# Kernel optimization log

Measured on AMD Instinct MI355X. Metric: run time of the kernel, lower is better.

Reference implementation:

```python
import jax, jax.numpy as jnp
import numpy as np
from jax import lax

B, C, H0, W0 = 8, 128, 62, 62
G, K, DIL, STRIDE, PAD = 4, 3, 1, 1, 1
P = K * K
GC = C // G
OFFSET_SCALE = 1.0


def setup_inputs() -> dict:
    key = jax.random.key(0)
    ks = jax.random.split(key, 10)
    s = 0.05
    return {
        "x": jax.random.normal(ks[0], (B, C, H0, W0), jnp.float32),
        "conv_w": jax.random.normal(ks[1], (C, C, 1, 1), jnp.float32) * s,
        "conv_b": jax.random.normal(ks[2], (C,), jnp.float32) * s,
        "in_proj_w": jax.random.normal(ks[3], (C, C), jnp.float32) * s,
        "in_proj_b": jnp.zeros((C,), jnp.float32),
        "dw_w": jax.random.normal(ks[4], (C, 1, K, K), jnp.float32) * s,
        "dw_b": jnp.zeros((C,), jnp.float32),
        "ln_g": jnp.ones((C,), jnp.float32),
        "ln_b": jnp.zeros((C,), jnp.float32),
        "off_w": jax.random.normal(ks[5], (C, G * P * 2), jnp.float32) * s,
        "off_b": jax.random.normal(ks[6], (G * P * 2,), jnp.float32) * s,
        "mask_w": jax.random.normal(ks[7], (C, G * P), jnp.float32) * s,
        "mask_b": jnp.zeros((G * P,), jnp.float32),
        "out_proj_w": jax.random.normal(ks[8], (C, C), jnp.float32) * s,
        "out_proj_b": jnp.zeros((C,), jnp.float32),
    }


def _bilinear_sample(img, ix, iy, Hp, Wp):
    # img: [B, G, Hp*Wp, GC] flattened spatial; ix, iy: [B, G, Q, P] pixel coords.
    # Matches torch grid_sample(bilinear, zeros, align_corners=False).
    x0 = jnp.floor(ix)
    y0 = jnp.floor(iy)

    def gather(xi, yi):
        valid = (xi >= 0) & (xi <= Wp - 1) & (yi >= 0) & (yi <= Hp - 1)
        xc = jnp.clip(xi, 0, Wp - 1).astype(jnp.int32)
        yc = jnp.clip(yi, 0, Hp - 1).astype(jnp.int32)
        lin = (yc * Wp + xc).reshape(img.shape[0], img.shape[1], -1)  # [B,G,Q*P]
        v = jnp.take_along_axis(img, lin[..., None], axis=2)          # [B,G,Q*P,GC]
        v = v.reshape(xi.shape + (img.shape[-1],))
        return v * valid[..., None].astype(img.dtype)

    wx1 = (ix - x0)[..., None]
    wx0 = 1.0 - wx1
    wy1 = (iy - y0)[..., None]
    wy0 = 1.0 - wy1
    return (gather(x0, y0) * wx0 * wy0
            + gather(x0 + 1.0, y0) * wx1 * wy0
            + gather(x0, y0 + 1.0) * wx0 * wy1
            + gather(x0 + 1.0, y0 + 1.0) * wx1 * wy1)


def _dcnv3_core(x_proj, offset, mask):
    # x_proj: [B,H,W,C] NHWC; offset: [B,H,W,G*P*2]; mask: [B,H,W,G*P] (softmaxed)
    Bn, H, W, _ = x_proj.shape
    xp = jnp.pad(x_proj, ((0, 0), (PAD, PAD), (PAD, PAD), (0, 0)))
    Hp, Wp = H + 2 * PAD, W + 2 * PAD  # H_out == H for K=3, PAD=1, STRIDE=1
    # reference points (normalized to padded size)
    ref_x = (jnp.arange(W, dtype=jnp.float32) * STRIDE + (DIL * (K - 1)) / 2.0 + 0.5) / Wp
    ref_y = (jnp.arange(H, dtype=jnp.float32) * STRIDE + (DIL * (K - 1)) / 2.0 + 0.5) / Hp
    ref = jnp.stack(jnp.broadcast_arrays(ref_x[None, :], ref_y[:, None]), -1)  # [H,W,2] (x,y)
    # dilation grid (same ordering as torch.meshgrid(x_lin, y_lin))
    klin = (jnp.arange(K, dtype=jnp.float32) * DIL - (DIL * (K - 1)) // 2)
    gx, gy = jnp.meshgrid(klin, klin, indexing='ij')
    grid = jnp.stack([gx / Wp, gy / Hp], -1).reshape(P, 2)
    grid = jnp.tile(grid[None], (G, 1, 1)).reshape(G * P, 2)
    spatial_norm = jnp.array([Wp, Hp], jnp.float32)
    loc = (ref[:, :, None, :] + grid[None, None] * OFFSET_SCALE)[None] \
        + offset.reshape(Bn, H, W, G * P, 2) * OFFSET_SCALE / spatial_norm
    g = 2.0 * loc - 1.0  # normalized grid in [-1,1]
    ix = ((g[..., 0] + 1.0) * Wp - 1.0) / 2.0  # align_corners=False unnormalize
    iy = ((g[..., 1] + 1.0) * Hp - 1.0) / 2.0
    Q = H * W
    ix = ix.reshape(Bn, Q, G, P).transpose(0, 2, 1, 3)  # [B,G,Q,P]
    iy = iy.reshape(Bn, Q, G, P).transpose(0, 2, 1, 3)
    img = xp.reshape(Bn, Hp * Wp, G, GC).transpose(0, 2, 1, 3)  # [B,G,S,GC]
    sampled = _bilinear_sample(img, ix, iy, Hp, Wp)             # [B,G,Q,P,GC]
    m = mask.reshape(Bn, Q, G, P).transpose(0, 2, 1, 3)
    out = jnp.einsum('bgqpc,bgqp->bqgc', sampled, m)
    return out.reshape(Bn, H, W, G * GC)


def reference(x, conv_w, conv_b, in_proj_w, in_proj_b, dw_w, dw_b, ln_g, ln_b,
              off_w, off_b, mask_w, mask_b, out_proj_w, out_proj_b):
    dn = ('NCHW', 'OIHW', 'NCHW')
    # 1x1 conv with padding=1 (spatial grows by 2 on each dim)
    y = lax.conv_general_dilated(x, conv_w, (1, 1), ((PAD, PAD), (PAD, PAD)),
                                 dimension_numbers=dn) + conv_b[None, :, None, None]
    t = y.transpose(0, 2, 3, 1)  # NHWC
    x_proj = t @ in_proj_w + in_proj_b
    # offset/mask branch: depthwise conv + LayerNorm + GELU
    d = lax.conv_general_dilated(y, dw_w, (1, 1), ((1, 1), (1, 1)),
                                 dimension_numbers=dn,
                                 feature_group_count=C) + dw_b[None, :, None, None]
    d = d.transpose(0, 2, 3, 1)
    mu = d.mean(-1, keepdims=True)
    var = ((d - mu) ** 2).mean(-1, keepdims=True)
    d = (d - mu) / jnp.sqrt(var + 1e-5) * ln_g + ln_b
    d = jax.nn.gelu(d, approximate=False)
    offset = d @ off_w + off_b
    Bn, H, W, _ = d.shape
    m = jax.nn.softmax((d @ mask_w + mask_b).reshape(Bn, H, W, G, P), axis=-1)
    out = _dcnv3_core(x_proj, offset, m.reshape(Bn, H, W, G * P))
    out = out @ out_proj_w + out_proj_b
    return out.transpose(0, 3, 1, 2)  # back to NCHW
```

## Files before the change

kernel.cpp:

```cpp
#include <hip/hip_runtime.h>
#include <math.h>

#define BB 8
#define CH 128
#define HH 64
#define WWID 64
#define HIN 62
#define WIN 62
#define SPIN (HIN*WIN)
#define HP 66
#define WP 66
#define GP2 70
#define GG 4
#define GCH 32
#define NPIX (BB*HH*WWID)
#define ASTRIDE 136
#define XPHALFS ((size_t)BB*GP2*GP2*CH)

typedef _Float16 v8h __attribute__((ext_vector_type(8)));
typedef _Float16 v4h __attribute__((ext_vector_type(4)));
typedef float    v4f __attribute__((ext_vector_type(4)));
typedef float    f4a __attribute__((ext_vector_type(4), aligned(4)));

__global__ __launch_bounds__(256) void p0_pack(const float* __restrict__ conv_w,
                                               const float* __restrict__ in_proj_w,
                                               const float* __restrict__ off_w,
                                               const float* __restrict__ mask_w,
                                               const float* __restrict__ out_proj_w,
                                               const float* __restrict__ dw_w,
                                               _Float16* __restrict__ wp,
                                               float* __restrict__ dwT,
                                               _Float16* __restrict__ xpad16) {
    int t = threadIdx.x;
    int blk = blockIdx.x;
    if (blk >= 32) {
        size_t nvec = XPHALFS / 8;
        for (size_t i = (size_t)(blk - 32) * 256 + t; i < nvec; i += 32 * 256)
            *(v8h*)&xpad16[i * 8] = (v8h)(_Float16)0;
        return;
    }
    if (blk == 31) {
        if (t < 128) {
            #pragma unroll
            for (int tap = 0; tap < 9; tap++) dwT[tap * 128 + t] = dw_w[t * 9 + tap];
        }
        return;
    }
    int tid = blk * 256 + t;
    int mat, base;
    if (tid < 2048)      { mat = 0; base = 0; }
    else if (tid < 4096) { mat = 1; base = 2048; }
    else if (tid < 5888) { mat = 2; base = 4096; }
    else                 { mat = 3; base = 5888; }
    int fi = tid - base;
    int nt = fi >> 8, rem = fi & 255, kc = rem >> 6, lane = rem & 63;
    int n = nt * 16 + (lane & 15);
    int kbase = kc * 32 + ((lane >> 4) & 3) * 8;
    _Float16* dst = wp + (size_t)tid * 8;
    #pragma unroll
    for (int j = 0; j < 8; j++) {
        int k = kbase + j;
        float v;
        if (mat == 0)      v = conv_w[n * CH + k];
        else if (mat == 1) v = in_proj_w[k * CH + n];
        else if (mat == 2) v = (n < 72) ? off_w[k * 72 + n]
                               : (n < 108 ? mask_w[k * 36 + (n - 72)] : 0.f);
        else               v = out_proj_w[k * CH + n];
        dst[j] = (_Float16)v;
    }
}

__device__ inline void mfma_loop8(const _Float16* __restrict__ a16,
                                  const _Float16* __restrict__ wp,
                                  v4f acc[4], int t) {
    int lane = t & 63;
    int wv = t >> 6;
    int mt = wv >> 1, ntb = (wv & 1) * 4;
    const _Float16* abase = a16 + (mt * 16 + (lane & 15)) * ASTRIDE + ((lane >> 4) * 8);
    #pragma unroll
    for (int kc = 0; kc < 4; kc++) {
        v8h av = *(const v8h*)(abase + kc * 32);
        #pragma unroll
        for (int j = 0; j < 4; j++) {
            v8h bv = *(const v8h*)(wp + ((size_t)((ntb + j) * 4 + kc) * 64 + lane) * 8);
            acc[j] = __builtin_amdgcn_mfma_f32_16x16x32_f16(av, bv, acc[j], 0, 0, 0);
        }
    }
}

__device__ inline void acc_to_a16_8(_Float16* a16, v4f acc[4], int t) {
    int lane = t & 63, ncol = lane & 15;
    int wv = t >> 6;
    int m0 = (wv >> 1) * 16 + ((lane >> 4) * 4);
    int ntb = (wv & 1) * 4;
    #pragma unroll
    for (int j = 0; j < 4; j++)
        #pragma unroll
        for (int r = 0; r < 4; r++)
            a16[(m0 + r) * ASTRIDE + (ntb + j) * 16 + ncol] = (_Float16)acc[j][r];
}

__global__ __launch_bounds__(512) void gA_conv_inproj(const float* __restrict__ x,
                                                      const _Float16* __restrict__ wp_conv,
                                                      const _Float16* __restrict__ wp_in,
                                                      const float* __restrict__ conv_b,
                                                      const float* __restrict__ in_b,
                                                      _Float16* __restrict__ y16,
                                                      _Float16* __restrict__ xpad16) {
    __shared__ _Float16 a16[64 * ASTRIDE];
    int pix0 = blockIdx.x * 64;
    int t = threadIdx.x;
    int h = (pix0 >> 6) & 63, b = pix0 >> 12;
    bool hin = (h >= 1 && h <= 62);
    for (int q = t; q < 2048; q += 512) {
        int c = q >> 4, w4 = (q & 15) * 4;
        float4 v = make_float4(0.f, 0.f, 0.f, 0.f);
        if (hin) {
            const float* xr = x + ((size_t)(b * CH + c)) * SPIN + (h - 1) * WIN;
            if (w4 == 0)       { f4a e = *(const f4a*)&xr[0];      v = make_float4(0.f, e[0], e[1], e[2]); }
            else if (w4 == 60) { f4a e = *(const f4a*)&xr[58];     v = make_float4(e[1], e[2], e[3], 0.f); }
            else               { f4a e = *(const f4a*)&xr[w4 - 1]; v = make_float4(e[0], e[1], e[2], e[3]); }
        }
        a16[(w4 + 0) * ASTRIDE + c] = (_Float16)v.x;
        a16[(w4 + 1) * ASTRIDE + c] = (_Float16)v.y;
        a16[(w4 + 2) * ASTRIDE + c] = (_Float16)v.z;
        a16[(w4 + 3) * ASTRIDE + c] = (_Float16)v.w;
    }
    __syncthreads();
    int lane = t & 63, ncol = lane & 15;
    int ntb = ((t >> 6) & 1) * 4;
    v4f acc[4];
    #pragma unroll
    for (int j = 0; j < 4; j++) {
        float bv = conv_b[(ntb + j) * 16 + ncol];
        acc[j] = (v4f){bv, bv, bv, bv};
    }
    mfma_loop8(a16, wp_conv, acc, t);
    __syncthreads();
    acc_to_a16_8(a16, acc, t);
    __syncthreads();
    {
        _Float16* dst = y16 + (size_t)pix0 * CH;
        for (int q = t; q < 1024; q += 512)
            *(v8h*)&dst[q * 8] = *(const v8h*)&a16[(q >> 4) * ASTRIDE + (q & 15) * 8];
    }
    v4f acc2[4];
    #pragma unroll
    for (int j = 0; j < 4; j++) {
        float bv = in_b[(ntb + j) * 16 + ncol];
        acc2[j] = (v4f){bv, bv, bv, bv};
    }
    mfma_loop8(a16, wp_in, acc2, t);
    __syncthreads();
    acc_to_a16_8(a16, acc2, t);
    __syncthreads();
    {
        _Float16* dst = xpad16 + (size_t)(((b * GP2) + h + 3) * GP2 + 3) * CH;
        for (int q = t; q < 1024; q += 512)
            *(v8h*)&dst[q * 8] = *(const v8h*)&a16[(q >> 4) * ASTRIDE + (q & 15) * 8];
    }
}

__global__ __launch_bounds__(512) void gF_dwln_offmask(const _Float16* __restrict__ y16,
                                                       const _Float16* __restrict__ wp_om,
                                                       const float* __restrict__ dwT,
                                                       const float* __restrict__ dw_b,
                                                       const float* __restrict__ ln_g,
                                                       const float* __restrict__ ln_b,
                                                       const float* __restrict__ off_b,
                                                       const float* __restrict__ mask_b,
                                                       float* __restrict__ tapmeta) {
    __shared__ char smem[49920];
    _Float16* ylds = (_Float16*)smem;
    int t = threadIdx.x;
    int pix0 = blockIdx.x * 64;
    int h = (pix0 >> 6) & 63, b = pix0 >> 12;
    if (h == 0 || h == 63) {
        for (int i = t; i < 3120; i += 512) *(v8h*)&ylds[i * 8] = (v8h)(_Float16)0;
        __syncthreads();
    }
    for (int idx = t; idx < 3072; idx += 512) {
        int r = idx >> 10, w = (idx >> 4) & 63, c8 = idx & 15;
        int hh = h + r - 1;
        if (hh >= 0 && hh <= 63) {
            v8h v = *(const v8h*)&y16[(size_t)(((b * 64 + hh) * 64 + w) * CH) + c8 * 8];
            *(v8h*)&ylds[(size_t)((r * 16 + c8) * 65 + w) * 8] = v;
        }
    }
    __syncthreads();
    int px = t >> 3, q8 = t & 7;
    float acc[16];
    #pragma unroll
    for (int cb = 0; cb < 4; cb++) *(float4*)&acc[cb * 4] = *(const float4*)&dw_b[q8 * 16 + cb * 4];
    #pragma unroll
    for (int r = 0; r < 3; r++) {
        #pragma unroll
        for (int kx = 0; kx < 3; kx++) {
            int wq = px + kx - 1;
            bool valid = (wq >= 0 && wq <= 63);
            int wpc = min(max(wq, 0), 63);
            int tap = r * 3 + kx;
            if (valid) {
                #pragma unroll
                for (int cb = 0; cb < 2; cb++) {
                    v8h yv = *(const v8h*)&ylds[(size_t)((r * 16 + q8 * 2 + cb) * 65 + wpc) * 8];
                    float4 wa = *(const float4*)&dwT[tap * 128 + q8 * 16 + cb * 8];
                    float4 wb = *(const float4*)&dwT[tap * 128 + q8 * 16 + cb * 8 + 4];
                    acc[cb*8+0] += (float)yv[0] * wa.x; acc[cb*8+1] += (float)yv[1] * wa.y;
                    acc[cb*8+2] += (float)yv[2] * wa.z; acc[cb*8+3] += (float)yv[3] * wa.w;
                    acc[cb*8+4] += (float)yv[4] * wb.x; acc[cb*8+5] += (float)yv[5] * wb.y;
                    acc[cb*8+6] += (float)yv[6] * wb.z; acc[cb*8+7] += (float)yv[7] * wb.w;
                }
            }
        }
    }
    float s = 0.f, ss = 0.f;
    #pragma unroll
    for (int j = 0; j < 16; j++) { s += acc[j]; ss += acc[j] * acc[j]; }
    s  += __shfl_xor(s, 1);  s  += __shfl_xor(s, 2);  s  += __shfl_xor(s, 4);
    ss += __shfl_xor(ss, 1); ss += __shfl_xor(ss, 2); ss += __shfl_xor(ss, 4);
    float mu = s * (1.f / 128.f);
    float var = ss * (1.f / 128.f) - mu * mu;
    float rstd = rsqrtf(var + 1e-5f);
    v8h dreg[2];
    #pragma unroll
    for (int cb = 0; cb < 2; cb++) {
        float4 ga = *(const float4*)&ln_g[q8 * 16 + cb * 8];
        float4 gb = *(const float4*)&ln_g[q8 * 16 + cb * 8 + 4];
        float4 ba = *(const float4*)&ln_b[q8 * 16 + cb * 8];
        float4 bb = *(const float4*)&ln_b[q8 * 16 + cb * 8 + 4];
        float gv[8] = {ga.x, ga.y, ga.z, ga.w, gb.x, gb.y, gb.z, gb.w};
        float bv[8] = {ba.x, ba.y, ba.z, ba.w, bb.x, bb.y, bb.z, bb.w};
        #pragma unroll
        for (int j = 0; j < 8; j++) {
            float xln = (acc[cb * 8 + j] - mu) * rstd * gv[j] + bv[j];
            float gel = 0.5f * xln * (1.f + erff(xln * 0.70710678118654752f));
            dreg[cb][j] = (_Float16)gel;
        }
    }
    __syncthreads();
    _Float16* a16 = (_Float16*)smem;
    float* om = (float*)(smem + 17408);
    #pragma unroll
    for (int cb = 0; cb < 2; cb++)
        *(v8h*)&a16[px * ASTRIDE + q8 * 16 + cb * 8] = dreg[cb];
    __syncthreads();
    int lane = t & 63, ncol = lane & 15;
    int ntb = ((t >> 6) & 1) * 4;
    v4f macc[4];
    #pragma unroll
    for (int j = 0; j < 4; j++) {
        int n = (ntb + j) * 16 + ncol;
        float bv = (n < 72) ? off_b[n] : (n < 108 ? mask_b[n - 72] : 0.f);
        macc[j] = (v4f){bv, bv, bv, bv};
    }
    mfma_loop8(a16, wp_om, macc, t);
    int m0 = ((t >> 6) >> 1) * 16 + ((lane >> 4) * 4);
    #pragma unroll
    for (int j = 0; j < 4; j++) {
        if (ntb + j < 7) {
            #pragma unroll
            for (int r = 0; r < 4; r++)
                om[(m0 + r) * 112 + (ntb + j) * 16 + ncol] = macc[j][r];
        }
    }
    __syncthreads();
    {
        int job = t >> 1, half = t & 1;
        int pxs = job >> 2, gx = job & 3;
        const float* row = &om[pxs * 112];
        float lg[9];
        #pragma unroll
        for (int i = 0; i < 9; i++) lg[i] = row[72 + gx * 9 + i];
        float mx = lg[0];
        #pragma unroll
        for (int i = 1; i < 9; i++) mx = fmaxf(mx, lg[i]);
        float e[9], sum = 0.f;
        #pragma unroll
        for (int i = 0; i < 9; i++) { e[i] = expf(lg[i] - mx); sum += e[i]; }
        float inv = 1.f / sum;
        float* tm = tapmeta + ((size_t)(pix0 + pxs) * 36 + gx * 9) * 4;
        int pstart = half * 5;
        int pcount = half ? 4 : 5;
        #pragma unroll
        for (int pp = 0; pp < 5; pp++) {
            if (pp >= pcount) break;
            int p = pstart + pp;
            int gp = gx * 9 + p;
            float offx = row[gp * 2];
            float offy = row[gp * 2 + 1];
            float m = e[p] * inv;
            float ix = (float)(pxs + (p / 3)) + offx;
            float iy = (float)(h + (p % 3)) + offy;
            ix = fminf(fmaxf(ix, -2.f), (float)(WP + 1));
            iy = fminf(fmaxf(iy, -2.f), (float)(HP + 1));
            float x0f = floorf(ix), y0f = floorf(iy);
            float fx = ix - x0f, fy = iy - y0f;
            int x0 = (int)x0f, y0 = (int)y0f;
            int off = ((y0 + 2) * GP2 + (x0 + 2)) * CH;
            float4 rec;
            rec.x = __int_as_float(off);
            rec.y = fx; rec.z = fy; rec.w = m;
            *(float4*)&tm[p * 4] = rec;
        }
    }
}

__global__ __launch_bounds__(256) void kD_gather(const _Float16* __restrict__ xpad16,
                                                 const float* __restrict__ tapmeta,
                                                 _Float16* __restrict__ core16) {
    __shared__ float meta[8 * 36 * 4];
    int t = threadIdx.x;
    int pix0 = blockIdx.x * 8;
    const float4* src = (const float4*)(tapmeta + (size_t)pix0 * 36 * 4);
    for (int i = t; i < 288; i += 256) ((float4*)meta)[i] = src[i];
    __syncthreads();
    int px_l = t >> 5, lane5 = t & 31;
    int c4 = lane5 * 4, g = lane5 >> 3;
    int pix = pix0 + px_l;
    int b = pix >> 12;
    const _Float16* base = xpad16 + (size_t)b * GP2 * GP2 * CH + c4;
    float a0 = 0.f, a1 = 0.f, a2 = 0.f, a3 = 0.f;
    #pragma unroll
    for (int p = 0; p < 9; p++) {
        float4 rec = *(const float4*)&meta[(size_t)(px_l * 36 + g * 9 + p) * 4];
        int off = __float_as_int(rec.x);
        float fx = rec.y, fy = rec.z, m = rec.w;
        float w11 = fx * fy;
        float w10 = fx - w11;
        float w01 = fy - w11;
        float w00 = 1.f - fx - fy + w11;
        w00 *= m; w10 *= m; w01 *= m; w11 *= m;
        v4h h0 = *(const v4h*)&base[off];
        v4h h1 = *(const v4h*)&base[off + CH];
        v4h h2 = *(const v4h*)&base[off + GP2 * CH];
        v4h h3 = *(const v4h*)&base[off + GP2 * CH + CH];
        a0 += w00*(float)h0[0] + w10*(float)h1[0] + w01*(float)h2[0] + w11*(float)h3[0];
        a1 += w00*(float)h0[1] + w10*(float)h1[1] + w01*(float)h2[1] + w11*(float)h3[1];
        a2 += w00*(float)h0[2] + w10*(float)h1[2] + w01*(float)h2[2] + w11*(float)h3[2];
        a3 += w00*(float)h0[3] + w10*(float)h1[3] + w01*(float)h2[3] + w11*(float)h3[3];
    }
    v4h res = { (_Float16)a0, (_Float16)a1, (_Float16)a2, (_Float16)a3 };
    *(v4h*)&core16[(size_t)pix * CH + c4] = res;
}

__global__ __launch_bounds__(512) void g4_outproj(const _Float16* __restrict__ core16,
                                                  const _Float16* __restrict__ wp,
                                                  const float* __restrict__ bias,
                                                  float* __restrict__ out) {
    __shared__ _Float16 a16[64 * ASTRIDE];
    __shared__ float res[128 * 68];
    int pix0 = blockIdx.x * 64;
    int t = threadIdx.x;
    const _Float16* src = core16 + (size_t)pix0 * CH;
    for (int q = t; q < 1024; q += 512)
        *(v8h*)&a16[(q >> 4) * ASTRIDE + (q & 15) * 8] = *(const v8h*)&src[q * 8];
    __syncthreads();
    int lane = t & 63, ncol = lane & 15;
    int ntb = ((t >> 6) & 1) * 4;
    v4f acc[4];
    #pragma unroll
    for (int j = 0; j < 4; j++) {
        float bv = bias[(ntb + j) * 16 + ncol];
        acc[j] = (v4f){bv, bv, bv, bv};
    }
    mfma_loop8(a16, wp, acc, t);
    int m0 = ((t >> 6) >> 1) * 16 + ((lane >> 4) * 4);
    #pragma unroll
    for (int j = 0; j < 4; j++)
        #pragma unroll
        for (int r = 0; r < 4; r++)
            res[((ntb + j) * 16 + ncol) * 68 + (m0 + r)] = acc[j][r];
    __syncthreads();
    int b = pix0 >> 12, h = (pix0 >> 6) & 63;
    for (int q = t; q < 2048; q += 512) {
        int cc = q >> 4, w4 = (q & 15) * 4;
        float4 o = *(const float4*)&res[cc * 68 + w4];
        *(float4*)&out[(size_t)((b * CH + cc) * HH + h) * WWID + w4] = o;
    }
}

extern "C" void kernel_launch(void* const* d_in, const int* in_sizes, int n_in,
                              void* d_out, int out_size, void* d_ws, size_t ws_size,
                              hipStream_t stream) {
    const float* x        = (const float*)d_in[0];
    const float* conv_w   = (const float*)d_in[1];
    const float* conv_b   = (const float*)d_in[2];
    const float* in_proj_w= (const float*)d_in[3];
    const float* in_proj_b= (const float*)d_in[4];
    const float* dw_w     = (const float*)d_in[5];
    const float* dw_b     = (const float*)d_in[6];
    const float* ln_g     = (const float*)d_in[7];
    const float* ln_b     = (const float*)d_in[8];
    const float* off_w    = (const float*)d_in[9];
    const float* off_b    = (const float*)d_in[10];
    const float* mask_w   = (const float*)d_in[11];
    const float* mask_b   = (const float*)d_in[12];
    const float* out_proj_w = (const float*)d_in[13];
    const float* out_proj_b = (const float*)d_in[14];
    float* out = (float*)d_out;

    float* ws = (float*)d_ws;
    const size_t O_WP   = 0;
    const size_t O_DWT  = 32768;
    const size_t O_Y16  = 34816;
    const size_t O_XP16 = O_Y16 + 2097152;
    const size_t O_C16  = O_XP16 + 2508800;
    const size_t O_TM   = O_C16 + 2097152;
    _Float16* wp     = (_Float16*)(ws + O_WP);
    float*    dwT    = ws + O_DWT;
    _Float16* y16    = (_Float16*)(ws + O_Y16);
    _Float16* xpad16 = (_Float16*)(ws + O_XP16);
    _Float16* core16 = (_Float16*)(ws + O_C16);
    float*    tapmeta= ws + O_TM;

    _Float16* wp_conv = wp;
    _Float16* wp_in   = wp + (size_t)2048 * 8;
    _Float16* wp_om   = wp + (size_t)4096 * 8;
    _Float16* wp_out  = wp + (size_t)5888 * 8;

    p0_pack<<<64, 256, 0, stream>>>(conv_w, in_proj_w, off_w, mask_w, out_proj_w, dw_w, wp, dwT, xpad16);
    gA_conv_inproj<<<NPIX / 64, 512, 0, stream>>>(x, wp_conv, wp_in, conv_b, in_proj_b, y16, xpad16);
    gF_dwln_offmask<<<NPIX / 64, 512, 0, stream>>>(y16, wp_om, dwT, dw_b, ln_g, ln_b, off_b, mask_b, tapmeta);
    kD_gather<<<NPIX / 8, 256, 0, stream>>>(xpad16, tapmeta, core16);
    g4_outproj<<<NPIX / 64, 512, 0, stream>>>(core16, wp_out, out_proj_b, out);
}
```

Baseline: 162.7 us.

## Fuse deformable gather with output projection in one kernel

Merges the bilinear gather kernel and the out-projection MFMA kernel into one kernel that handles 16 pixels per 128-thread block. The sampled core values stay in shared memory as fp16 and feed the MFMA directly, so the core16 intermediate is never written to or read back from global memory and one launch disappears. Each thread now gathers 16 channels with 8-wide vector loads instead of 4, which cuts the number of load instructions. In exchange, each block reloads the full out-projection weights for only 16 pixels, and the output stores become 64-byte row segments rather than full 256-byte rows.

```diff
diff --git a/kernel.cpp b/kernel.cpp
--- a/kernel.cpp
+++ b/kernel.cpp
@@ -306,77 +306,93 @@
     }
 }
 
-__global__ __launch_bounds__(256) void kD_gather(const _Float16* __restrict__ xpad16,
-                                                 const float* __restrict__ tapmeta,
-                                                 _Float16* __restrict__ core16) {
-    __shared__ float meta[8 * 36 * 4];
+__global__ __launch_bounds__(128) void gG_gather_outproj(const _Float16* __restrict__ xpad16,
+                                                         const float* __restrict__ tapmeta,
+                                                         const _Float16* __restrict__ wp,
+                                                         const float* __restrict__ bias,
+                                                         float* __restrict__ out) {
+    __shared__ char smem[14592];
+    _Float16* a16 = (_Float16*)smem;
+    float* meta = (float*)(smem + 4352);
+    float* res  = (float*)(smem + 4352);
     int t = threadIdx.x;
-    int pix0 = blockIdx.x * 8;
-    const float4* src = (const float4*)(tapmeta + (size_t)pix0 * 36 * 4);
-    for (int i = t; i < 288; i += 256) ((float4*)meta)[i] = src[i];
-    __syncthreads();
-    int px_l = t >> 5, lane5 = t & 31;
-    int c4 = lane5 * 4, g = lane5 >> 3;
-    int pix = pix0 + px_l;
-    int b = pix >> 12;
-    const _Float16* base = xpad16 + (size_t)b * GP2 * GP2 * CH + c4;
-    float a0 = 0.f, a1 = 0.f, a2 = 0.f, a3 = 0.f;
-    #pragma unroll
-    for (int p = 0; p < 9; p++) {
-        float4 rec = *(const float4*)&meta[(size_t)(px_l * 36 + g * 9 + p) * 4];
-        int off = __float_as_int(rec.x);
-        float fx = rec.y, fy = rec.z, m = rec.w;
-        float w11 = fx * fy;
-        float w10 = fx - w11;
-        float w01 = fy - w11;
-        float w00 = 1.f - fx - fy + w11;
-        w00 *= m; w10 *= m; w01 *= m; w11 *= m;
-        v4h h0 = *(const v4h*)&base[off];
-        v4h h1 = *(const v4h*)&base[off + CH];
-        v4h h2 = *(const v4h*)&base[off + GP2 * CH];
-        v4h h3 = *(const v4h*)&base[off + GP2 * CH + CH];
-        a0 += w00*(float)h0[0] + w10*(float)h1[0] + w01*(float)h2[0] + w11*(float)h3[0];
-        a1 += w00*(float)h0[1] + w10*(float)h1[1] + w01*(float)h2[1] + w11*(float)h3[1];
-        a2 += w00*(float)h0[2] + w10*(float)h1[2] + w01*(float)h2[2] + w11*(float)h3[2];
-        a3 += w00*(float)h0[3] + w10*(float)h1[3] + w01*(float)h2[3] + w11*(float)h3[3];
-    }
-    v4h res = { (_Float16)a0, (_Float16)a1, (_Float16)a2, (_Float16)a3 };
-    *(v4h*)&core16[(size_t)pix * CH + c4] = res;
-}
-
-__global__ __launch_bounds__(512) void g4_outproj(const _Float16* __restrict__ core16,
-                                                  const _Float16* __restrict__ wp,
-                                                  const float* __restrict__ bias,
-                                                  float* __restrict__ out) {
-    __shared__ _Float16 a16[64 * ASTRIDE];
-    __shared__ float res[128 * 68];
-    int pix0 = blockIdx.x * 64;
-    int t = threadIdx.x;
-    const _Float16* src = core16 + (size_t)pix0 * CH;
-    for (int q = t; q < 1024; q += 512)
-        *(v8h*)&a16[(q >> 4) * ASTRIDE + (q & 15) * 8] = *(const v8h*)&src[q * 8];
+    int pix0 = blockIdx.x * 16;
+    int b = pix0 >> 12, h = (pix0 >> 6) & 63, wbase = pix0 & 63;
+    {
+        const float4* src = (const float4*)(tapmeta + (size_t)pix0 * 36 * 4);
+        for (int i = t; i < 576; i += 128) ((float4*)meta)[i] = src[i];
+    }
+    __syncthreads();
+    {
+        int px_l = t >> 3, s = t & 7;
+        int ch = s * 16, g = s >> 1;
+        const _Float16* base = xpad16 + (size_t)b * GP2 * GP2 * CH + ch;
+        const float* tmb = &meta[(size_t)(px_l * 36 + g * 9) * 4];
+        float acc[16];
+        #pragma unroll
+        for (int j = 0; j < 16; j++) acc[j] = 0.f;
+        #pragma unroll
+        for (int p = 0; p < 9; p++) {
+            float4 rec = *(const float4*)&tmb[p * 4];
+            int off = __float_as_int(rec.x);
+            float fx = rec.y, fy = rec.z, m = rec.w;
+            float w11 = fx * fy;
+            float w10 = fx - w11;
+            float w01 = fy - w11;
+            float w00 = 1.f - fx - fy + w11;
+            w00 *= m; w10 *= m; w01 *= m; w11 *= m;
+            v8h c0a = *(const v8h*)&base[off];
+            v8h c0b = *(const v8h*)&base[off + 8];
+            v8h c1a = *(const v8h*)&base[off + CH];
+            v8h c1b = *(const v8h*)&base[off + CH + 8];
+            v8h c2a = *(const v8h*)&base[off + GP2 * CH];
+            v8h c2b = *(const v8h*)&base[off + GP2 * CH + 8];
+            v8h c3a = *(const v8h*)&base[off + GP2 * CH + CH];
+            v8h c3b = *(const v8h*)&base[off + GP2 * CH + CH + 8];
+            #pragma unroll
+            for (int j = 0; j < 8; j++) {
+                acc[j]     += w00*(float)c0a[j] + w10*(float)c1a[j] + w01*(float)c2a[j] + w11*(float)c3a[j];
+                acc[j + 8] += w00*(float)c0b[j] + w10*(float)c1b[j] + w01*(float)c2b[j] + w11*(float)c3b[j];
+            }
+        }
+        v8h r0, r1;
+        #pragma unroll
+        for (int j = 0; j < 8; j++) { r0[j] = (_Float16)acc[j]; r1[j] = (_Float16)acc[j + 8]; }
+        *(v8h*)&a16[px_l * ASTRIDE + ch]     = r0;
+        *(v8h*)&a16[px_l * ASTRIDE + ch + 8] = r1;
+    }
     __syncthreads();
     int lane = t & 63, ncol = lane & 15;
-    int ntb = ((t >> 6) & 1) * 4;
-    v4f acc[4];
+    int ntb = (t >> 6) * 4;
+    v4f macc[4];
     #pragma unroll
     for (int j = 0; j < 4; j++) {
         float bv = bias[(ntb + j) * 16 + ncol];
-        acc[j] = (v4f){bv, bv, bv, bv};
-    }
-    mfma_loop8(a16, wp, acc, t);
-    int m0 = ((t >> 6) >> 1) * 16 + ((lane >> 4) * 4);
+        macc[j] = (v4f){bv, bv, bv, bv};
+    }
+    {
+        const _Float16* abase = a16 + (lane & 15) * ASTRIDE + ((lane >> 4) * 8);
+        #pragma unroll
+        for (int kc = 0; kc < 4; kc++) {
+            v8h av = *(const v8h*)(abase + kc * 32);
+            #pragma unroll
+            for (int j = 0; j < 4; j++) {
+                v8h bv = *(const v8h*)(wp + ((size_t)((ntb + j) * 4 + kc) * 64 + lane) * 8);
+                macc[j] = __builtin_amdgcn_mfma_f32_16x16x32_f16(av, bv, macc[j], 0, 0, 0);
+            }
+        }
+    }
+    int m0 = (lane >> 4) * 4;
     #pragma unroll
     for (int j = 0; j < 4; j++)
         #pragma unroll
         for (int r = 0; r < 4; r++)
-            res[((ntb + j) * 16 + ncol) * 68 + (m0 + r)] = acc[j][r];
-    __syncthreads();
-    int b = pix0 >> 12, h = (pix0 >> 6) & 63;
-    for (int q = t; q < 2048; q += 512) {
-        int cc = q >> 4, w4 = (q & 15) * 4;
-        float4 o = *(const float4*)&res[cc * 68 + w4];
-        *(float4*)&out[(size_t)((b * CH + cc) * HH + h) * WWID + w4] = o;
+            res[((ntb + j) * 16 + ncol) * 20 + (m0 + r)] = macc[j][r];
+    __syncthreads();
+    for (int q = t; q < 512; q += 128) {
+        int cc = q >> 2, w4 = (q & 3) * 4;
+        float4 o = *(const float4*)&res[cc * 20 + w4];
+        *(float4*)&out[(size_t)((b * CH + cc) * HH + h) * WWID + wbase + w4] = o;
     }
 }
 
@@ -405,13 +421,11 @@
     const size_t O_DWT  = 32768;
     const size_t O_Y16  = 34816;
     const size_t O_XP16 = O_Y16 + 2097152;
-    const size_t O_C16  = O_XP16 + 2508800;
-    const size_t O_TM   = O_C16 + 2097152;
+    const size_t O_TM   = O_XP16 + 2508800;
     _Float16* wp     = (_Float16*)(ws + O_WP);
     float*    dwT    = ws + O_DWT;
     _Float16* y16    = (_Float16*)(ws + O_Y16);
     _Float16* xpad16 = (_Float16*)(ws + O_XP16);
-    _Float16* core16 = (_Float16*)(ws + O_C16);
     float*    tapmeta= ws + O_TM;
 
     _Float16* wp_conv = wp;
@@ -422,6 +436,5 @@
     p0_pack<<<64, 256, 0, stream>>>(conv_w, in_proj_w, off_w, mask_w, out_proj_w, dw_w, wp, dwT, xpad16);
     gA_conv_inproj<<<NPIX / 64, 512, 0, stream>>>(x, wp_conv, wp_in, conv_b, in_proj_b, y16, xpad16);
     gF_dwln_offmask<<<NPIX / 64, 512, 0, stream>>>(y16, wp_om, dwT, dw_b, ln_g, ln_b, off_b, mask_b, tapmeta);
-    kD_gather<<<NPIX / 8, 256, 0, stream>>>(xpad16, tapmeta, core16);
-    g4_outproj<<<NPIX / 64, 512, 0, stream>>>(core16, wp_out, out_proj_b, out);
-}
+    gG_gather_outproj<<<NPIX / 16, 128, 0, stream>>>(xpad16, tapmeta, wp_out, out_proj_b, out);
+}
```

Result: slower. 174.7 us (+7.4%).
